# Performance work log

Hardware: AMD Instinct MI355X
Metric: run time of the kernel (lower is better)

## Reference

```python
import jax, jax.numpy as jnp
import numpy as np

N_NODES = 50000


def setup_inputs() -> dict:
    key = jax.random.key(0)
    k1, k2, k3, k4, k5 = jax.random.split(key, 5)
    d_in, d_out, n_edges = 128, 128, 800000
    x = jax.random.normal(k1, (N_NODES, d_in), dtype=jnp.float32)
    edge_index = jax.random.randint(k2, (2, n_edges), 0, N_NODES, dtype=jnp.int64)
    # Glorot-ish init for linear weights, bias zeros-like small normal
    W_l = jax.random.normal(k3, (d_in, d_out), dtype=jnp.float32) / np.sqrt(d_in)
    W_r = jax.random.normal(k4, (d_in, d_out), dtype=jnp.float32) / np.sqrt(d_in)
    b = jax.random.normal(k5, (d_out,), dtype=jnp.float32) * 0.01
    return {"x": x, "edge_index": edge_index, "W_l": W_l, "W_r": W_r, "b": b}


def reference(x, edge_index, W_l, W_r, b):
    # PyG SAGEConv (aggr='mean', root_weight=True, bias=True):
    #   out_i = W_l @ mean_{j: (j->i) in E} x_j + b + W_r @ x_i
    # followed by ReLU (GConv act) and dropout(p=0.0, eval) == identity.
    src, dst = edge_index[0], edge_index[1]
    msgs = x[src]                                            # [E, d_in] gather
    agg_sum = jax.ops.segment_sum(msgs, dst, num_segments=N_NODES)  # [N, d_in]
    deg = jax.ops.segment_sum(jnp.ones_like(dst, dtype=x.dtype), dst,
                              num_segments=N_NODES)          # [N]
    agg_mean = agg_sum / jnp.maximum(deg, 1.0)[:, None]      # zero for isolated nodes
    z = agg_mean @ W_l + b + x @ W_r                         # [N, d_out]
    return jax.nn.relu(z)
```

## Files before the change

### kernel.cpp

```cpp
#include <hip/hip_runtime.h>

#define N_NODES 50000
#define D 128
#define NC 256
#define SCANB 196
#define CONV_NB 1563
#define ZROW 50000

typedef short bf16x8 __attribute__((ext_vector_type(8)));
typedef float f32x4 __attribute__((ext_vector_type(4)));
typedef float f32x2 __attribute__((ext_vector_type(2)));
typedef unsigned char uchar;

__device__ __forceinline__ ushort f2bf(float f) {
    uint u = __float_as_uint(f);
    u += 0x7FFF + ((u >> 16) & 1);
    return (ushort)(u >> 16);
}

__device__ __forceinline__ void addrow8(uint2 q, float* a) {
    f32x2 p;
    p = __builtin_amdgcn_cvt_pk_f32_fp8(q.x, false); a[0] += p.x; a[1] += p.y;
    p = __builtin_amdgcn_cvt_pk_f32_fp8(q.x, true);  a[2] += p.x; a[3] += p.y;
    p = __builtin_amdgcn_cvt_pk_f32_fp8(q.y, false); a[4] += p.x; a[5] += p.y;
    p = __builtin_amdgcn_cvt_pk_f32_fp8(q.y, true);  a[6] += p.x; a[7] += p.y;
}

__device__ __forceinline__ void scan_base(const int* __restrict__ blocksums,
                                          int* base, int* wtot) {
    const int t = threadIdx.x;
    const int lane = t & 63;
    const int wid = t >> 6;
    int v = (t < SCANB) ? blocksums[t] : 0;
    int sc = v;
    #pragma unroll
    for (int off = 1; off < 64; off <<= 1) {
        int u = __shfl_up(sc, off);
        if (lane >= off) sc += u;
    }
    if (t < 256 && lane == 63) wtot[wid] = sc;
    __syncthreads();
    if (t < SCANB) {
        int wb = 0;
        #pragma unroll
        for (int w2 = 0; w2 < 4; ++w2) if (w2 < wid) wb += wtot[w2];
        base[t] = wb + sc - v;
    }
    __syncthreads();
}

__global__ __launch_bounds__(1024) void fused_count_convert(
        const float* __restrict__ x, const float* __restrict__ Wl,
        const float* __restrict__ Wr, const int* __restrict__ dst,
        ushort* __restrict__ x_bf, int* __restrict__ x_fp8,
        ushort* __restrict__ Btf, uchar* __restrict__ cum,
        uint* __restrict__ sorted_u32,
        int E, int chunk) {
    const int b = blockIdx.x;
    const int t = threadIdx.x;
    if (b < NC) {
        __shared__ uint cnt[N_NODES / 4];
        for (int k = t; k < N_NODES / 4; k += 1024) cnt[k] = 0;
        __syncthreads();
        const int e0 = b * chunk;
        const int e1 = min(E, e0 + chunk);
        for (int e = e0 + t; e < e1; e += 1024) {
            int d = dst[e];
            atomicAdd(&cnt[d >> 2], 1u << ((d & 3) << 3));
        }
        __syncthreads();
        uint* pu = (uint*)(cum + (size_t)b * N_NODES);
        for (int k = t; k < N_NODES / 4; k += 1024) pu[k] = cnt[k];
    } else {
        const int i = (b - NC) * 1024 + t;
        if (i < (N_NODES * D) / 4) {
            float4 v = ((const float4*)x)[i];
            ushort4 o;
            o.x = f2bf(v.x); o.y = f2bf(v.y); o.z = f2bf(v.z); o.w = f2bf(v.w);
            ((ushort4*)x_bf)[i] = o;
            int p = __builtin_amdgcn_cvt_pk_fp8_f32(v.x, v.y, 0, false);
            p = __builtin_amdgcn_cvt_pk_fp8_f32(v.z, v.w, p, true);
            x_fp8[i] = p;
        }
        if (i < 600008) sorted_u32[i] = 0xC350C350u;
        if (i < 32) x_fp8[ZROW * 32 + i] = 0;
        if (i < 32768) {
            int j  = i & 7;
            int l  = (i >> 3) & 63;
            int nf = (i >> 9) & 7;
            int ks = (i >> 12) & 7;
            int lr = l & 15, kb = l >> 4;
            int col  = nf * 16 + lr;
            int kloc = (ks & 3) * 32 + kb * 8 + j;
            const float* W = (ks < 4) ? Wl : Wr;
            Btf[i] = f2bf(W[kloc * D + col]);
        }
    }
}

__global__ __launch_bounds__(256) void scanAB_kernel(uchar* __restrict__ cum,
                                                     int* __restrict__ offsetsP,
                                                     int* __restrict__ blocksums,
                                                     ushort* __restrict__ degArr) {
    __shared__ int wsums[4];
    __shared__ int wbase[4];
    const int t = threadIdx.x;
    const int lane = t & 63;
    const int wid = t >> 6;
    const int n = blockIdx.x * 256 + t;

    int s = 0;
    if (n < N_NODES) {
        #pragma unroll 4
        for (int c = 0; c < NC; ++c) {
            int v = (int)cum[(size_t)c * N_NODES + n];
            cum[(size_t)c * N_NODES + n] = (uchar)s;
            s += v;
        }
        degArr[n] = (ushort)s;
    }
    const int sp = (s + 7) & ~7;
    int sc = sp;
    #pragma unroll
    for (int off = 1; off < 64; off <<= 1) {
        int u = __shfl_up(sc, off);
        if (lane >= off) sc += u;
    }
    if (lane == 63) wsums[wid] = sc;
    __syncthreads();
    if (t == 0) {
        int c = 0;
        #pragma unroll
        for (int w = 0; w < 4; ++w) { int tmp = wsums[w]; wbase[w] = c; c += tmp; }
        blocksums[blockIdx.x] = c;
    }
    __syncthreads();
    if (n < N_NODES) offsetsP[n] = wbase[wid] + sc - sp;
}

__global__ __launch_bounds__(1024) void scatterC_kernel(const int* __restrict__ src,
                                                        const int* __restrict__ dst,
                                                        const int* __restrict__ offsetsP,
                                                        const int* __restrict__ blocksums,
                                                        const uchar* __restrict__ cum,
                                                        ushort* __restrict__ sorted_src,
                                                        int E, int chunk) {
    __shared__ uint cnt[N_NODES / 4];
    __shared__ int base[SCANB];
    __shared__ int wtot[4];
    const int t = threadIdx.x;
    const int b = blockIdx.x;
    for (int k = t; k < N_NODES / 4; k += 1024) cnt[k] = 0;
    scan_base(blocksums, base, wtot);
    const uchar* cb = cum + (size_t)b * N_NODES;
    const int e0 = b * chunk;
    const int e1 = min(E, e0 + chunk);
    for (int e = e0 + t; e < e1; e += 1024) {
        int d = dst[e];
        uint prev = atomicAdd(&cnt[d >> 2], 1u << ((d & 3) << 3));
        int lrank = (int)((prev >> ((d & 3) << 3)) & 0xFFu);
        int pos = offsetsP[d] + base[d >> 8] + (int)cb[d] + lrank;
        sorted_src[pos] = (ushort)src[e];
    }
}

__global__ __launch_bounds__(256) void aggregate_fp8(const int* __restrict__ x_fp8,
                                                     const ushort* __restrict__ sorted_src,
                                                     const int* __restrict__ offsetsP,
                                                     const int* __restrict__ blocksums,
                                                     const ushort* __restrict__ degArr,
                                                     ushort* __restrict__ agg_bf) {
    __shared__ int base[SCANB];
    __shared__ int wtot[4];
    const int b = blockIdx.x;
    const int t = threadIdx.x;

    scan_base(blocksums, base, wtot);

    const int g = t >> 4;
    const int j = t & 15;
    const int node = b * 16 + g;
    if (node >= N_NODES) return;
    const int dg = (int)degArr[node];
    const int s = offsetsP[node] + base[node >> 8];
    const int npad = (dg + 7) & ~7;

    const uint2* xq = (const uint2*)x_fp8;

    float a[8];
    #pragma unroll
    for (int k = 0; k < 8; ++k) a[k] = 0.0f;

    const int pend = s + npad;
    for (int p = s; p < pend; p += 8) {
        uint4 qi = *(const uint4*)&sorted_src[p];
        int s0 = qi.x & 0xFFFF, s1 = qi.x >> 16;
        int s2 = qi.y & 0xFFFF, s3 = qi.y >> 16;
        int s4 = qi.z & 0xFFFF, s5 = qi.z >> 16;
        int s6 = qi.w & 0xFFFF, s7 = qi.w >> 16;
        uint2 q0 = xq[s0 * 16 + j];
        uint2 q1 = xq[s1 * 16 + j];
        uint2 q2 = xq[s2 * 16 + j];
        uint2 q3 = xq[s3 * 16 + j];
        uint2 q4 = xq[s4 * 16 + j];
        uint2 q5 = xq[s5 * 16 + j];
        uint2 q6 = xq[s6 * 16 + j];
        uint2 q7 = xq[s7 * 16 + j];
        addrow8(q0, a); addrow8(q1, a); addrow8(q2, a); addrow8(q3, a);
        addrow8(q4, a); addrow8(q5, a); addrow8(q6, a); addrow8(q7, a);
    }

    const float scale = (dg > 0) ? (1.0f / (float)dg) : 0.0f;
    ushort tmp[8];
    #pragma unroll
    for (int k = 0; k < 8; ++k) tmp[k] = f2bf(a[k] * scale);
    *(int4*)&agg_bf[node * D + j * 8] = *(int4*)tmp;
}

__global__ __launch_bounds__(256) void gemm_direct(const ushort* __restrict__ agg_bf,
                                                   const ushort* __restrict__ x_bf,
                                                   const ushort* __restrict__ Btf,
                                                   const float* __restrict__ bias,
                                                   float* __restrict__ out) {
    const int t = threadIdx.x;
    const int w = t >> 6;
    const int l = t & 63;
    const int lr = l & 15;
    const int kb = l >> 4;
    const int n0 = blockIdx.x * 64;

    int r = n0 + w * 16 + lr;
    if (r >= N_NODES) r = N_NODES - 1;

    f32x4 acc[8] = {};

    #pragma unroll
    for (int ks = 0; ks < 8; ++ks) {
        bf16x8 af = (ks < 4)
            ? *(const bf16x8*)&agg_bf[r * D + ks * 32 + kb * 8]
            : *(const bf16x8*)&x_bf[r * D + (ks - 4) * 32 + kb * 8];
        const ushort* bp = Btf + (size_t)(ks * 8 * 64 + l) * 8;
        #pragma unroll
        for (int nf = 0; nf < 8; ++nf) {
            bf16x8 bfr = *(const bf16x8*)&bp[nf * 64 * 8];
            acc[nf] = __builtin_amdgcn_mfma_f32_16x16x32_bf16(af, bfr, acc[nf], 0, 0, 0);
        }
    }

    #pragma unroll
    for (int nf = 0; nf < 8; ++nf) {
        const int col = nf * 16 + lr;
        const float bb = bias[col];
        #pragma unroll
        for (int i = 0; i < 4; ++i) {
            int row = n0 + w * 16 + kb * 4 + i;
            if (row < N_NODES)
                out[row * D + col] = fmaxf(acc[nf][i] + bb, 0.0f);
        }
    }
}

extern "C" void kernel_launch(void* const* d_in, const int* in_sizes, int n_in,
                              void* d_out, int out_size, void* d_ws, size_t ws_size,
                              hipStream_t stream) {
    const float* x  = (const float*)d_in[0];
    const int*   ei = (const int*)d_in[1];
    const float* Wl = (const float*)d_in[2];
    const float* Wr = (const float*)d_in[3];
    const float* b  = (const float*)d_in[4];
    float* out = (float*)d_out;

    const int E = in_sizes[1] / 2;
    const int* src = ei;
    const int* dst = ei + E;
    const int chunk = (E + NC - 1) / NC;

    char* wsp = (char*)d_ws;
    int*    offsetsP  = (int*)(wsp + 0);
    int*    blocksums = (int*)(wsp + 200704);
    ushort* degArr    = (ushort*)(wsp + 201728);
    ushort* sorted    = (ushort*)(wsp + 301760);
    uchar*  cum       = (uchar*)(wsp + 2701792);
    ushort* x_bf      = (ushort*)(wsp + 15501792);
    int*    x_fp8     = (int*)(wsp + 28301792);
    ushort* agg_bf    = (ushort*)(wsp + 34701920);
    ushort* Btf       = (ushort*)(wsp + 47501920);

    fused_count_convert<<<NC + CONV_NB, 1024, 0, stream>>>(
        x, Wl, Wr, dst, x_bf, x_fp8, Btf, cum, (uint*)sorted, E, chunk);
    scanAB_kernel<<<SCANB, 256, 0, stream>>>(cum, offsetsP, blocksums, degArr);
    scatterC_kernel<<<NC, 1024, 0, stream>>>(src, dst, offsetsP, blocksums, cum,
                                             sorted, E, chunk);
    aggregate_fp8<<<(N_NODES + 15) / 16, 256, 0, stream>>>(
        x_fp8, sorted, offsetsP, blocksums, degArr, agg_bf);
    gemm_direct<<<(N_NODES + 63) / 64, 256, 0, stream>>>(agg_bf, x_bf, Btf, b, out);
}
```

Before: 96.36 us.

## Merge scan+scatter and aggregate+gemm into cooperative kernels with grid sync

Replaces the four separate launches after the count kernel with two cooperative launches. Each one uses a grid-wide sync between phases: scan then scatter, and aggregate then GEMM. The GEMM phase uses persistent grid-stride loops. The scan is reshaped into 49 blocks of 1024 threads, each handling four 256-node chunks. The aim is to cut kernel launch gaps and the per-block blocksum prefix recomputation. In exchange it adds grid-sync cost, limits the grid to co-resident blocks, and falls back to separate launches if the cooperative launch fails.

Result: slower. 133.5 us (+38.5%).

```diff
diff --git a/kernel.cpp b/kernel.cpp
--- a/kernel.cpp
+++ b/kernel.cpp
@@ -1,4 +1,6 @@
 #include <hip/hip_runtime.h>
+#include <hip/hip_cooperative_groups.h>
+namespace cg = cooperative_groups;
 
 #define N_NODES 50000
 #define D 128
@@ -6,6 +8,8 @@
 #define SCANB 196
 #define CONV_NB 1563
 #define ZROW 50000
+#define AGG_TILES 3125
+#define GEMM_TILES 782
 
 typedef short bf16x8 __attribute__((ext_vector_type(8)));
 typedef float f32x4 __attribute__((ext_vector_type(4)));
@@ -98,16 +102,16 @@
     }
 }
 
-__global__ __launch_bounds__(256) void scanAB_kernel(uchar* __restrict__ cum,
-                                                     int* __restrict__ offsetsP,
-                                                     int* __restrict__ blocksums,
-                                                     ushort* __restrict__ degArr) {
-    __shared__ int wsums[4];
-    __shared__ int wbase[4];
-    const int t = threadIdx.x;
-    const int lane = t & 63;
-    const int wid = t >> 6;
-    const int n = blockIdx.x * 256 + t;
+__device__ void scan_phase_body(uchar* __restrict__ cum, int* __restrict__ offsetsP,
+                                int* __restrict__ blocksums, ushort* __restrict__ degArr,
+                                int b) {
+    __shared__ int wsums[4][4];
+    const int t = threadIdx.x;
+    const int chunkId = t >> 8;
+    const int ct = t & 255;
+    const int lane = ct & 63;
+    const int wid = ct >> 6;
+    const int n = b * 1024 + t;
 
     int s = 0;
     if (n < N_NODES) {
@@ -126,30 +130,28 @@
         int u = __shfl_up(sc, off);
         if (lane >= off) sc += u;
     }
-    if (lane == 63) wsums[wid] = sc;
+    if (lane == 63) wsums[chunkId][wid] = sc;
     __syncthreads();
-    if (t == 0) {
-        int c = 0;
-        #pragma unroll
-        for (int w = 0; w < 4; ++w) { int tmp = wsums[w]; wbase[w] = c; c += tmp; }
-        blocksums[blockIdx.x] = c;
-    }
-    __syncthreads();
-    if (n < N_NODES) offsetsP[n] = wbase[wid] + sc - sp;
-}
-
-__global__ __launch_bounds__(1024) void scatterC_kernel(const int* __restrict__ src,
-                                                        const int* __restrict__ dst,
-                                                        const int* __restrict__ offsetsP,
-                                                        const int* __restrict__ blocksums,
-                                                        const uchar* __restrict__ cum,
-                                                        ushort* __restrict__ sorted_src,
-                                                        int E, int chunk) {
+    int wb = 0;
+    #pragma unroll
+    for (int w2 = 0; w2 < 4; ++w2) if (w2 < wid) wb += wsums[chunkId][w2];
+    const int grp = 4 * b + chunkId;
+    if (ct == 0 && grp < SCANB)
+        blocksums[grp] = wsums[chunkId][0] + wsums[chunkId][1]
+                       + wsums[chunkId][2] + wsums[chunkId][3];
+    if (n < N_NODES) offsetsP[n] = wb + sc - sp;
+}
+
+__device__ void scatter_phase_body(const int* __restrict__ src, const int* __restrict__ dst,
+                                   const int* __restrict__ offsetsP,
+                                   const int* __restrict__ blocksums,
+                                   const uchar* __restrict__ cum,
+                                   ushort* __restrict__ sorted_src,
+                                   int E, int chunk, int b) {
     __shared__ uint cnt[N_NODES / 4];
     __shared__ int base[SCANB];
     __shared__ int wtot[4];
     const int t = threadIdx.x;
-    const int b = blockIdx.x;
     for (int k = t; k < N_NODES / 4; k += 1024) cnt[k] = 0;
     scan_base(blocksums, base, wtot);
     const uchar* cb = cum + (size_t)b * N_NODES;
@@ -164,22 +166,16 @@
     }
 }
 
-__global__ __launch_bounds__(256) void aggregate_fp8(const int* __restrict__ x_fp8,
-                                                     const ushort* __restrict__ sorted_src,
-                                                     const int* __restrict__ offsetsP,
-                                                     const int* __restrict__ blocksums,
-                                                     const ushort* __restrict__ degArr,
-                                                     ushort* __restrict__ agg_bf) {
-    __shared__ int base[SCANB];
-    __shared__ int wtot[4];
-    const int b = blockIdx.x;
-    const int t = threadIdx.x;
-
-    scan_base(blocksums, base, wtot);
-
+__device__ void aggregate_body(const int* __restrict__ x_fp8,
+                               const ushort* __restrict__ sorted_src,
+                               const int* __restrict__ offsetsP,
+                               const ushort* __restrict__ degArr,
+                               ushort* __restrict__ agg_bf,
+                               const int* base, int vb) {
+    const int t = threadIdx.x;
     const int g = t >> 4;
     const int j = t & 15;
-    const int node = b * 16 + g;
+    const int node = vb * 16 + g;
     if (node >= N_NODES) return;
     const int dg = (int)degArr[node];
     const int s = offsetsP[node] + base[node >> 8];
@@ -217,23 +213,21 @@
     *(int4*)&agg_bf[node * D + j * 8] = *(int4*)tmp;
 }
 
-__global__ __launch_bounds__(256) void gemm_direct(const ushort* __restrict__ agg_bf,
-                                                   const ushort* __restrict__ x_bf,
-                                                   const ushort* __restrict__ Btf,
-                                                   const float* __restrict__ bias,
-                                                   float* __restrict__ out) {
+__device__ void gemm_body(const ushort* __restrict__ agg_bf,
+                          const ushort* __restrict__ x_bf,
+                          const ushort* __restrict__ Btf,
+                          const float* __restrict__ bias,
+                          float* __restrict__ out, int n0) {
     const int t = threadIdx.x;
     const int w = t >> 6;
     const int l = t & 63;
     const int lr = l & 15;
     const int kb = l >> 4;
-    const int n0 = blockIdx.x * 64;
 
     int r = n0 + w * 16 + lr;
     if (r >= N_NODES) r = N_NODES - 1;
 
     f32x4 acc[8] = {};
-
     #pragma unroll
     for (int ks = 0; ks < 8; ++ks) {
         bf16x8 af = (ks < 4)
@@ -246,7 +240,6 @@
             acc[nf] = __builtin_amdgcn_mfma_f32_16x16x32_bf16(af, bfr, acc[nf], 0, 0, 0);
         }
     }
-
     #pragma unroll
     for (int nf = 0; nf < 8; ++nf) {
         const int col = nf * 16 + lr;
@@ -260,6 +253,55 @@
     }
 }
 
+__global__ __launch_bounds__(1024) void coopA_kernel(uchar* cum, int* offsetsP,
+                                                     int* blocksums, ushort* degArr,
+                                                     const int* src, const int* dst,
+                                                     ushort* sorted_src, int E, int chunk) {
+    const int b = blockIdx.x;
+    if (b < 49) scan_phase_body(cum, offsetsP, blocksums, degArr, b);
+    cg::this_grid().sync();
+    scatter_phase_body(src, dst, offsetsP, blocksums, cum, sorted_src, E, chunk, b);
+}
+
+__global__ __launch_bounds__(256) void coopB_kernel(const int* x_fp8, const ushort* sorted_src,
+                                                    const int* offsetsP, const int* blocksums,
+                                                    const ushort* degArr, ushort* agg_bf,
+                                                    const ushort* x_bf, const ushort* Btf,
+                                                    const float* bias, float* out) {
+    __shared__ int base[SCANB];
+    __shared__ int wtot[4];
+    scan_base(blocksums, base, wtot);
+    for (int vb = blockIdx.x; vb < AGG_TILES; vb += gridDim.x)
+        aggregate_body(x_fp8, sorted_src, offsetsP, degArr, agg_bf, base, vb);
+    cg::this_grid().sync();
+    for (int vb = blockIdx.x; vb < GEMM_TILES; vb += gridDim.x)
+        gemm_body(agg_bf, x_bf, Btf, bias, out, vb * 64);
+}
+
+__global__ __launch_bounds__(1024) void scan_fb(uchar* cum, int* offsetsP,
+                                                int* blocksums, ushort* degArr) {
+    scan_phase_body(cum, offsetsP, blocksums, degArr, blockIdx.x);
+}
+__global__ __launch_bounds__(1024) void scatter_fb(const int* src, const int* dst,
+                                                   const int* offsetsP, const int* blocksums,
+                                                   const uchar* cum, ushort* sorted_src,
+                                                   int E, int chunk) {
+    scatter_phase_body(src, dst, offsetsP, blocksums, cum, sorted_src, E, chunk, blockIdx.x);
+}
+__global__ __launch_bounds__(256) void agg_fb(const int* x_fp8, const ushort* sorted_src,
+                                              const int* offsetsP, const int* blocksums,
+                                              const ushort* degArr, ushort* agg_bf) {
+    __shared__ int base[SCANB];
+    __shared__ int wtot[4];
+    scan_base(blocksums, base, wtot);
+    aggregate_body(x_fp8, sorted_src, offsetsP, degArr, agg_bf, base, blockIdx.x);
+}
+__global__ __launch_bounds__(256) void gemm_fb(const ushort* agg_bf, const ushort* x_bf,
+                                               const ushort* Btf, const float* bias,
+                                               float* out) {
+    gemm_body(agg_bf, x_bf, Btf, bias, out, blockIdx.x * 64);
+}
+
 extern "C" void kernel_launch(void* const* d_in, const int* in_sizes, int n_in,
                               void* d_out, int out_size, void* d_ws, size_t ws_size,
                               hipStream_t stream) {
@@ -267,7 +309,7 @@
     const int*   ei = (const int*)d_in[1];
     const float* Wl = (const float*)d_in[2];
     const float* Wr = (const float*)d_in[3];
-    const float* b  = (const float*)d_in[4];
+    const float* bias = (const float*)d_in[4];
     float* out = (float*)d_out;
 
     const int E = in_sizes[1] / 2;
@@ -288,10 +330,41 @@
 
     fused_count_convert<<<NC + CONV_NB, 1024, 0, stream>>>(
         x, Wl, Wr, dst, x_bf, x_fp8, Btf, cum, (uint*)sorted, E, chunk);
-    scanAB_kernel<<<SCANB, 256, 0, stream>>>(cum, offsetsP, blocksums, degArr);
-    scatterC_kernel<<<NC, 1024, 0, stream>>>(src, dst, offsetsP, blocksums, cum,
-                                             sorted, E, chunk);
-    aggregate_fp8<<<(N_NODES + 15) / 16, 256, 0, stream>>>(
-        x_fp8, sorted, offsetsP, blocksums, degArr, agg_bf);
-    gemm_direct<<<(N_NODES + 63) / 64, 256, 0, stream>>>(agg_bf, x_bf, Btf, b, out);
-}
+
+    {
+        uchar* a0 = cum; int* a1 = offsetsP; int* a2 = blocksums; ushort* a3 = degArr;
+        const int* a4 = src; const int* a5 = dst; ushort* a6 = sorted;
+        int a7 = E, a8 = chunk;
+        void* argsA[] = {&a0, &a1, &a2, &a3, &a4, &a5, &a6, &a7, &a8};
+        hipError_t eA = hipLaunchCooperativeKernel((void*)coopA_kernel, dim3(NC), dim3(1024),
+                                                   argsA, 0, stream);
+        if (eA != hipSuccess) {
+            scan_fb<<<49, 1024, 0, stream>>>(cum, offsetsP, blocksums, degArr);
+            scatter_fb<<<NC, 1024, 0, stream>>>(src, dst, offsetsP, blocksums, cum,
+                                                sorted, E, chunk);
+        }
+    }
+
+    {
+        int perCU = 0;
+        hipError_t eq = hipOccupancyMaxActiveBlocksPerMultiprocessor(
+            &perCU, (const void*)coopB_kernel, 256, 0);
+        int gridB = (eq == hipSuccess && perCU > 0) ? perCU * 256 : 0;
+        if (gridB > AGG_TILES) gridB = AGG_TILES;
+        hipError_t eB = hipErrorUnknown;
+        if (gridB > 0) {
+            const int* b0 = x_fp8; const ushort* b1 = sorted; const int* b2 = offsetsP;
+            const int* b3 = blocksums; const ushort* b4 = degArr; ushort* b5 = agg_bf;
+            const ushort* b6 = x_bf; const ushort* b7 = Btf; const float* b8 = bias;
+            float* b9 = out;
+            void* argsB[] = {&b0, &b1, &b2, &b3, &b4, &b5, &b6, &b7, &b8, &b9};
+            eB = hipLaunchCooperativeKernel((void*)coopB_kernel, dim3(gridB), dim3(256),
+                                            argsB, 0, stream);
+        }
+        if (eB != hipSuccess) {
+            agg_fb<<<AGG_TILES, 256, 0, stream>>>(x_fp8, sorted, offsetsP, blocksums,
+                                                  degArr, agg_bf);
+            gemm_fb<<<GEMM_TILES, 256, 0, stream>>>(agg_bf, x_bf, Btf, bias, out);
+        }
+    }
+}
```
